# Optimization experiments

Hardware: AMD Instinct MI355X
Metric: run time of the kernel (lower is better)

## Reference

```python
import jax, jax.numpy as jnp
import numpy as np

MAX_ITER = 10
TAU = 1.0


def setup_inputs() -> dict:
    key = jax.random.key(0)
    k1, k2, k3 = jax.random.split(key, 3)
    B, R, C = 64, 1024, 1024
    s = jax.random.normal(k1, (B, R, C), dtype=jnp.float32)
    # nrows <= ncols per batch => no transposed_batch branch in the original
    nrows = jax.random.randint(k2, (B,), 128, 512).astype(jnp.int32)
    ncols = jax.random.randint(k3, (B,), 512, C + 1).astype(jnp.int32)
    return {"s": s, "nrows": nrows, "ncols": ncols}


def _masked_lse(x, mask, axis):
    """logsumexp over `axis` restricted to mask==True; finite-safe everywhere.
    Equivalent to torch.logsumexp after writing -inf into masked-out entries,
    but keeps all values finite so grads are clean."""
    neg = jnp.asarray(-1e30, x.dtype)
    m = jax.lax.stop_gradient(jnp.max(jnp.where(mask, x, neg), axis=axis, keepdims=True))
    e = jnp.where(mask, jnp.exp(jnp.where(mask, x, m) - m), jnp.zeros((), x.dtype))
    sum_e = jnp.sum(e, axis=axis, keepdims=True)
    any_m = jnp.any(mask, axis=axis, keepdims=True)
    return m + jnp.log(jnp.where(any_m, sum_e, jnp.ones((), x.dtype)))


def _sinkhorn(s, nrows, ncols):
    B, R, C = s.shape
    row_mask = (jnp.arange(R)[None, :] < nrows[:, None])[:, :, None]  # [B,R,1]
    col_mask = (jnp.arange(C)[None, :] < ncols[:, None])[:, None, :]  # [B,1,C]
    valid = row_mask & col_mask                                        # [B,R,C]
    log_s = s / TAU
    # Alternating row/col normalization in log space. In the original, entries
    # outside [nrows,ncols] are set to -inf and ignored by logsumexp; here we
    # keep them finite and mask inside the logsumexp, which is the same math
    # on the valid region, and we zero the invalid region at the end (exp(-inf)=0).
    for i in range(MAX_ITER):
        if i % 2 == 0:  # row normalization
            lse = _masked_lse(log_s, valid, axis=2)          # [B,R,1]
            log_s = log_s - jnp.where(row_mask, lse, 0.0)
        else:           # col normalization
            lse = _masked_lse(log_s, valid, axis=1)          # [B,1,C]
            log_s = log_s - jnp.where(col_mask, lse, 0.0)
    return jnp.where(valid, jnp.exp(log_s), jnp.zeros((), s.dtype))


def reference(s, nrows, ncols):
    return _sinkhorn(s, nrows, ncols)
```

## Files before the change

kernel.cpp:

```cpp
#include <hip/hip_runtime.h>
#include <hip/hip_fp16.h>


#define B_DIM 64

__device__ __forceinline__ float fast_rcp(float x) {
#if __has_builtin(__builtin_amdgcn_rcpf)
    return __builtin_amdgcn_rcpf(x);
#else
    return 1.0f / x;
#endif
}


__global__ __launch_bounds__(256) void pack_row0(
    const float* __restrict__ s, const int* __restrict__ nrows,
    const int* __restrict__ ncols, __half* __restrict__ E,
    float* __restrict__ a, float* __restrict__ cs0)
{
    const int b = blockIdx.y;
    const int t = threadIdx.x;
    if (blockIdx.x == 0) {
        #pragma unroll
        for (int k = 0; k < 4; ++k) cs0[(b << 10) + (k << 8) + t] = 0.f;
    }
    const int r = (blockIdx.x << 2) + (t >> 6);
    const int nr = nrows[b];
    if (r >= nr) return;
    const int lane = t & 63;
    const int nc = ncols[b];
    const float* __restrict__ srow = s + ((size_t)b << 20) + ((size_t)r << 10);
    __half* __restrict__ erow = E + ((size_t)b << 19) + ((size_t)r << 10);

    float sum = 0.f;
    #pragma unroll
    for (int k = 0; k < 4; ++k) {
        const int c = (k << 8) + (lane << 2);
        const float4 x = *reinterpret_cast<const float4*>(srow + c);
        const float e0 = __expf(x.x), e1 = __expf(x.y),
                    e2 = __expf(x.z), e3 = __expf(x.w);
        float2 pk;
        reinterpret_cast<__half2*>(&pk)[0] = __floats2half2_rn(e0, e1);
        reinterpret_cast<__half2*>(&pk)[1] = __floats2half2_rn(e2, e3);
        *reinterpret_cast<float2*>(erow + c) = pk;
        sum += (c + 0 < nc ? e0 : 0.f) + (c + 1 < nc ? e1 : 0.f)
             + (c + 2 < nc ? e2 : 0.f) + (c + 3 < nc ? e3 : 0.f);
    }
    #pragma unroll
    for (int off = 1; off < 64; off <<= 1) sum += __shfl_xor(sum, off);
    if (lane == 0) a[(b << 9) + r] = 1.0f / sum;
}

__global__ __launch_bounds__(256) void row_step_f(
    const __half* __restrict__ E, const int* __restrict__ nrows,
    const int* __restrict__ ncols, const float* __restrict__ cs_prev,
    float* __restrict__ cs_zero, float* __restrict__ a)
{
    const int b = blockIdx.y;
    const int t = threadIdx.x;
    if (blockIdx.x == 0) {
        #pragma unroll
        for (int k = 0; k < 4; ++k) cs_zero[(b << 10) + (k << 8) + t] = 0.f;
    }
    const int r = (blockIdx.x << 2) + (t >> 6);
    const int nr = nrows[b];
    if (r >= nr) return;
    const int lane = t & 63;
    const int nc = ncols[b];
    const __half* __restrict__ erow = E + ((size_t)b << 19) + ((size_t)r << 10);
    const float* __restrict__ csb = cs_prev + (b << 10);

    float sum = 0.f;
    #pragma unroll
    for (int k = 0; k < 4; ++k) {
        const int c = (k << 8) + (lane << 2);
        float2 pk = *reinterpret_cast<const float2*>(erow + c);
        const float2 f01 = __half22float2(reinterpret_cast<const __half2*>(&pk)[0]);
        const float2 f23 = __half22float2(reinterpret_cast<const __half2*>(&pk)[1]);
        const float4 cs = *reinterpret_cast<const float4*>(csb + c);
        const float w0 = (c + 0 < nc) ? fast_rcp(cs.x) : 0.f;
        const float w1 = (c + 1 < nc) ? fast_rcp(cs.y) : 0.f;
        const float w2 = (c + 2 < nc) ? fast_rcp(cs.z) : 0.f;
        const float w3 = (c + 3 < nc) ? fast_rcp(cs.w) : 0.f;
        sum += f01.x * w0 + f01.y * w1 + f23.x * w2 + f23.y * w3;
    }
    #pragma unroll
    for (int off = 1; off < 64; off <<= 1) sum += __shfl_xor(sum, off);
    if (lane == 0) a[(b << 9) + r] = 1.0f / sum;
}

__global__ __launch_bounds__(256) void col_step_f(
    const __half* __restrict__ E, const int* __restrict__ nrows,
    const int* __restrict__ ncols, const float* __restrict__ a,
    float* __restrict__ cs_out)
{
    const int b = blockIdx.z;
    const int nr = nrows[b];
    const int r0 = blockIdx.y << 6;
    if (r0 >= nr) return;
    const int nc = ncols[b];
    const int c0 = (blockIdx.x << 9) + (threadIdx.x << 1);
    if (c0 >= nc) return;
    const int rend = min(r0 + 64, nr);

    const __half* __restrict__ Eb = E + ((size_t)b << 19) + c0;
    const float* __restrict__ ab = a + (b << 9);

    float sA0 = 0.f, sA1 = 0.f, sB0 = 0.f, sB1 = 0.f;
    int r = r0;
    for (; r + 4 <= rend; r += 4) {
        const float2 f0 = __half22float2(*reinterpret_cast<const __half2*>(Eb + ((size_t)(r + 0) << 10)));
        const float2 f1 = __half22float2(*reinterpret_cast<const __half2*>(Eb + ((size_t)(r + 1) << 10)));
        const float2 f2 = __half22float2(*reinterpret_cast<const __half2*>(Eb + ((size_t)(r + 2) << 10)));
        const float2 f3 = __half22float2(*reinterpret_cast<const __half2*>(Eb + ((size_t)(r + 3) << 10)));
        const float a0 = ab[r + 0], a1 = ab[r + 1], a2 = ab[r + 2], a3 = ab[r + 3];
        sA0 = fmaf(f0.x, a0, sA0); sA1 = fmaf(f0.y, a0, sA1);
        sB0 = fmaf(f1.x, a1, sB0); sB1 = fmaf(f1.y, a1, sB1);
        sA0 = fmaf(f2.x, a2, sA0); sA1 = fmaf(f2.y, a2, sA1);
        sB0 = fmaf(f3.x, a3, sB0); sB1 = fmaf(f3.y, a3, sB1);
    }
    for (; r < rend; ++r) {
        const float2 f = __half22float2(*reinterpret_cast<const __half2*>(Eb + ((size_t)r << 10)));
        const float av = ab[r];
        sA0 = fmaf(f.x, av, sA0); sA1 = fmaf(f.y, av, sA1);
    }
    atomicAdd(cs_out + (b << 10) + c0, sA0 + sB0);
    if (c0 + 1 < nc)
        atomicAdd(cs_out + (b << 10) + c0 + 1, sA1 + sB1);
}

__global__ __launch_bounds__(256) void out_step_f(
    const __half* __restrict__ E, const int* __restrict__ nrows,
    const int* __restrict__ ncols, const float* __restrict__ a,
    const float* __restrict__ cs, float* __restrict__ out)
{
    const int g = (blockIdx.x << 8) + threadIdx.x;
    const int b = g >> 18;
    const int rem = g & 262143;
    const int r = rem >> 8;
    const int c0 = (rem & 255) << 2;
    const int nr = nrows[b];
    const int nc = ncols[b];
    float4 o = make_float4(0.f, 0.f, 0.f, 0.f);
    if (r < nr && c0 < nc) {
        const float ar = a[(b << 9) + r];
        float2 pk = *reinterpret_cast<const float2*>(
            E + ((size_t)b << 19) + ((size_t)r << 10) + c0);
        const float2 f01 = __half22float2(reinterpret_cast<const __half2*>(&pk)[0]);
        const float2 f23 = __half22float2(reinterpret_cast<const __half2*>(&pk)[1]);
        const float4 c4 = *reinterpret_cast<const float4*>(cs + (b << 10) + c0);
        o.x = f01.x * ar * fast_rcp(c4.x);
        o.y = (c0 + 1 < nc) ? f01.y * ar * fast_rcp(c4.y) : 0.f;
        o.z = (c0 + 2 < nc) ? f23.x * ar * fast_rcp(c4.z) : 0.f;
        o.w = (c0 + 3 < nc) ? f23.y * ar * fast_rcp(c4.w) : 0.f;
    }
    reinterpret_cast<float4*>(out)[g] = o;
}


__global__ __launch_bounds__(256) void row_step_lg(
    const float* __restrict__ s, const int* __restrict__ nrows,
    const int* __restrict__ ncols, const float* __restrict__ vlog,
    const int use_v, float* __restrict__ u)
{
    const int b = blockIdx.y, r = blockIdx.x;
    const int nr = nrows[b];
    if (r >= nr) return;
    const int nc = ncols[b];
    const int t = threadIdx.x, c0 = t << 2;
    float sum = 0.f;
    if (c0 < nc) {
        const float4 x = reinterpret_cast<const float4*>(
            s + ((size_t)b << 20) + ((size_t)r << 10))[t];
        float4 vv = make_float4(0.f, 0.f, 0.f, 0.f);
        if (use_v) vv = reinterpret_cast<const float4*>(vlog + ((size_t)b << 10))[t];
        sum  = (c0 + 0 < nc) ? __expf(x.x - vv.x) : 0.f;
        sum += (c0 + 1 < nc) ? __expf(x.y - vv.y) : 0.f;
        sum += (c0 + 2 < nc) ? __expf(x.z - vv.z) : 0.f;
        sum += (c0 + 3 < nc) ? __expf(x.w - vv.w) : 0.f;
    }
    #pragma unroll
    for (int off = 1; off < 64; off <<= 1) sum += __shfl_xor(sum, off);
    __shared__ float ss[4];
    if ((t & 63) == 0) ss[t >> 6] = sum;
    __syncthreads();
    if (t == 0) u[((size_t)b << 9) + r] = __logf(ss[0] + ss[1] + ss[2] + ss[3]);
}

__global__ __launch_bounds__(256) void col_step_lg(
    const float* __restrict__ s, const int* __restrict__ nrows,
    const int* __restrict__ ncols, const float* __restrict__ u,
    float* __restrict__ partial)
{
    const int b = blockIdx.z, rc = blockIdx.y;
    const int nr = nrows[b];
    const int r0 = rc << 6;
    if (r0 >= nr) return;
    const int nc = ncols[b];
    const int c = (blockIdx.x << 8) + threadIdx.x;
    float sum = 0.f;
    if (c < nc) {
        const int rend = min(r0 + 64, nr);
        const float* __restrict__ sb = s + ((size_t)b << 20) + c;
        const float* __restrict__ ub = u + ((size_t)b << 9);
        float s0 = 0.f, s1 = 0.f, s2 = 0.f, s3 = 0.f;
        int r = r0;
        for (; r + 4 <= rend; r += 4) {
            s0 += __expf(sb[(size_t)(r + 0) << 10] - ub[r + 0]);
            s1 += __expf(sb[(size_t)(r + 1) << 10] - ub[r + 1]);
            s2 += __expf(sb[(size_t)(r + 2) << 10] - ub[r + 2]);
            s3 += __expf(sb[(size_t)(r + 3) << 10] - ub[r + 3]);
        }
        for (; r < rend; ++r) s0 += __expf(sb[(size_t)r << 10] - ub[r]);
        sum = (s0 + s1) + (s2 + s3);
    }
    partial[(((size_t)b << 3) + rc) << 10 | c] = sum;
}

__global__ __launch_bounds__(256) void col_fin_lg(
    const int* __restrict__ nrows, const float* __restrict__ partial,
    float* __restrict__ vlog)
{
    const int idx = (blockIdx.x << 8) + threadIdx.x;
    const int b = idx >> 10;
    const int nch = (nrows[b] + 63) >> 6;
    const float* __restrict__ p = partial + ((size_t)(b << 3) << 10) + (idx & 1023);
    float sum = 0.f;
    for (int k = 0; k < nch; ++k) sum += p[(size_t)k << 10];
    vlog[idx] = (sum > 0.f) ? __logf(sum) : 0.f;
}

__global__ __launch_bounds__(256) void out_step_lg(
    const float* __restrict__ s, const int* __restrict__ nrows,
    const int* __restrict__ ncols, const float* __restrict__ u,
    const float* __restrict__ vlog, float* __restrict__ out)
{
    const size_t total4 = (size_t)B_DIM * 1024 * 1024 / 4;
    float4* out4 = reinterpret_cast<float4*>(out);
    const float4* s4 = reinterpret_cast<const float4*>(s);
    for (size_t i = (size_t)blockIdx.x * blockDim.x + threadIdx.x; i < total4;
         i += (size_t)gridDim.x * blockDim.x) {
        const int b = (int)(i >> 18);
        const int rem = (int)(i & 262143);
        const int r = rem >> 8;
        const int c0 = (rem & 255) << 2;
        const int nr = nrows[b], nc = ncols[b];
        float4 o;
        if (r >= nr || c0 >= nc) {
            o = make_float4(0.f, 0.f, 0.f, 0.f);
        } else {
            float4 x = s4[i];
            const float ur = u[((size_t)b << 9) + r];
            const float* vb = vlog + ((size_t)b << 10);
            o.x = (c0 + 0 < nc) ? __expf(x.x - ur - vb[c0 + 0]) : 0.f;
            o.y = (c0 + 1 < nc) ? __expf(x.y - ur - vb[c0 + 1]) : 0.f;
            o.z = (c0 + 2 < nc) ? __expf(x.z - ur - vb[c0 + 2]) : 0.f;
            o.w = (c0 + 3 < nc) ? __expf(x.w - ur - vb[c0 + 3]) : 0.f;
        }
        out4[i] = o;
    }
}


extern "C" void kernel_launch(void* const* d_in, const int* in_sizes, int n_in,
                              void* d_out, int out_size, void* d_ws, size_t ws_size,
                              hipStream_t stream) {
    const float* s = (const float*)d_in[0];
    const int* nrows = (const int*)d_in[1];
    const int* ncols = (const int*)d_in[2];
    float* out = (float*)d_out;

    const size_t E_BYTES = (size_t)B_DIM * 512 * 1024 * 2;
    const size_t NEED = E_BYTES + (size_t)B_DIM * 512 * 4 + 2 * (size_t)B_DIM * 1024 * 4;

    if (ws_size >= NEED) {
        __half* E = (__half*)d_ws;
        float* a = (float*)((char*)d_ws + E_BYTES);
        float* cs0 = a + B_DIM * 512;
        float* cs1 = cs0 + B_DIM * 1024;
        float* cs[2] = {cs0, cs1};

        const dim3 rowGrid(128, B_DIM);
        const dim3 colGrid(2, 8, B_DIM);
        pack_row0<<<rowGrid, 256, 0, stream>>>(s, nrows, ncols, E, a, cs0);
        col_step_f<<<colGrid, 256, 0, stream>>>(E, nrows, ncols, a, cs0);
        for (int i = 1; i < 5; ++i) {
            row_step_f<<<rowGrid, 256, 0, stream>>>(E, nrows, ncols,
                                                    cs[(i - 1) & 1], cs[i & 1], a);
            col_step_f<<<colGrid, 256, 0, stream>>>(E, nrows, ncols, a, cs[i & 1]);
        }
        out_step_f<<<65536, 256, 0, stream>>>(E, nrows, ncols, a, cs0, out);
    } else {
        float* u = (float*)d_ws;
        float* vlog = u + (size_t)B_DIM * 512;
        float* partial = vlog + (size_t)B_DIM * 1024;
        const dim3 rowGrid(512, B_DIM);
        const dim3 colGrid(4, 8, B_DIM);
        for (int it = 0; it < 5; ++it) {
            row_step_lg<<<rowGrid, 256, 0, stream>>>(s, nrows, ncols, vlog, it, u);
            col_step_lg<<<colGrid, 256, 0, stream>>>(s, nrows, ncols, u, partial);
            col_fin_lg<<<256, 256, 0, stream>>>(nrows, partial, vlog);
        }
        out_step_lg<<<4096, 256, 0, stream>>>(s, nrows, ncols, u, vlog, out);
    }
}
```

Before: 187.1 us.

## Fuse row and column Sinkhorn steps into one kernel per iteration pair

Merges each row-normalization kernel with the following column-sum kernel, so one block owns a 64-row chunk. It computes the row scales into LDS, then does the column partial sums with atomics from those rows, which it is likely to still find in cache. A third column-sum buffer and a memset rotate the zeroing so each launch clears the buffer for the next step. This halves the launch count, but the grid shrinks to 8x64 blocks of 512 threads, which may leave the GPU underoccupied.

```diff
diff --git a/kernel.cpp b/kernel.cpp
--- a/kernel.cpp
+++ b/kernel.cpp
@@ -12,99 +12,22 @@
 #endif
 }
 
-
-__global__ __launch_bounds__(256) void pack_row0(
-    const float* __restrict__ s, const int* __restrict__ nrows,
-    const int* __restrict__ ncols, __half* __restrict__ E,
-    float* __restrict__ a, float* __restrict__ cs0)
-{
-    const int b = blockIdx.y;
-    const int t = threadIdx.x;
-    if (blockIdx.x == 0) {
-        #pragma unroll
-        for (int k = 0; k < 4; ++k) cs0[(b << 10) + (k << 8) + t] = 0.f;
-    }
-    const int r = (blockIdx.x << 2) + (t >> 6);
-    const int nr = nrows[b];
-    if (r >= nr) return;
-    const int lane = t & 63;
-    const int nc = ncols[b];
-    const float* __restrict__ srow = s + ((size_t)b << 20) + ((size_t)r << 10);
-    __half* __restrict__ erow = E + ((size_t)b << 19) + ((size_t)r << 10);
-
-    float sum = 0.f;
+__device__ __forceinline__ float wave_sum(float x) {
     #pragma unroll
-    for (int k = 0; k < 4; ++k) {
-        const int c = (k << 8) + (lane << 2);
-        const float4 x = *reinterpret_cast<const float4*>(srow + c);
-        const float e0 = __expf(x.x), e1 = __expf(x.y),
-                    e2 = __expf(x.z), e3 = __expf(x.w);
-        float2 pk;
-        reinterpret_cast<__half2*>(&pk)[0] = __floats2half2_rn(e0, e1);
-        reinterpret_cast<__half2*>(&pk)[1] = __floats2half2_rn(e2, e3);
-        *reinterpret_cast<float2*>(erow + c) = pk;
-        sum += (c + 0 < nc ? e0 : 0.f) + (c + 1 < nc ? e1 : 0.f)
-             + (c + 2 < nc ? e2 : 0.f) + (c + 3 < nc ? e3 : 0.f);
-    }
-    #pragma unroll
-    for (int off = 1; off < 64; off <<= 1) sum += __shfl_xor(sum, off);
-    if (lane == 0) a[(b << 9) + r] = 1.0f / sum;
-}
-
-__global__ __launch_bounds__(256) void row_step_f(
-    const __half* __restrict__ E, const int* __restrict__ nrows,
-    const int* __restrict__ ncols, const float* __restrict__ cs_prev,
-    float* __restrict__ cs_zero, float* __restrict__ a)
-{
-    const int b = blockIdx.y;
-    const int t = threadIdx.x;
-    if (blockIdx.x == 0) {
-        #pragma unroll
-        for (int k = 0; k < 4; ++k) cs_zero[(b << 10) + (k << 8) + t] = 0.f;
-    }
-    const int r = (blockIdx.x << 2) + (t >> 6);
-    const int nr = nrows[b];
-    if (r >= nr) return;
-    const int lane = t & 63;
-    const int nc = ncols[b];
-    const __half* __restrict__ erow = E + ((size_t)b << 19) + ((size_t)r << 10);
-    const float* __restrict__ csb = cs_prev + (b << 10);
-
-    float sum = 0.f;
-    #pragma unroll
-    for (int k = 0; k < 4; ++k) {
-        const int c = (k << 8) + (lane << 2);
-        float2 pk = *reinterpret_cast<const float2*>(erow + c);
-        const float2 f01 = __half22float2(reinterpret_cast<const __half2*>(&pk)[0]);
-        const float2 f23 = __half22float2(reinterpret_cast<const __half2*>(&pk)[1]);
-        const float4 cs = *reinterpret_cast<const float4*>(csb + c);
-        const float w0 = (c + 0 < nc) ? fast_rcp(cs.x) : 0.f;
-        const float w1 = (c + 1 < nc) ? fast_rcp(cs.y) : 0.f;
-        const float w2 = (c + 2 < nc) ? fast_rcp(cs.z) : 0.f;
-        const float w3 = (c + 3 < nc) ? fast_rcp(cs.w) : 0.f;
-        sum += f01.x * w0 + f01.y * w1 + f23.x * w2 + f23.y * w3;
-    }
-    #pragma unroll
-    for (int off = 1; off < 64; off <<= 1) sum += __shfl_xor(sum, off);
-    if (lane == 0) a[(b << 9) + r] = 1.0f / sum;
-}
-
-__global__ __launch_bounds__(256) void col_step_f(
-    const __half* __restrict__ E, const int* __restrict__ nrows,
-    const int* __restrict__ ncols, const float* __restrict__ a,
-    float* __restrict__ cs_out)
-{
-    const int b = blockIdx.z;
-    const int nr = nrows[b];
-    const int r0 = blockIdx.y << 6;
+    for (int off = 1; off < 64; off <<= 1) x += __shfl_xor(x, off);
+    return x;
+}
+
+
+__device__ __forceinline__ void phase2_col(
+    const __half* __restrict__ E, const float* a_lds, int b, int r0, int nr,
+    int nc, int t, float* __restrict__ cs_cur)
+{
     if (r0 >= nr) return;
-    const int nc = ncols[b];
-    const int c0 = (blockIdx.x << 9) + (threadIdx.x << 1);
+    const int c0 = t << 1;
     if (c0 >= nc) return;
     const int rend = min(r0 + 64, nr);
-
     const __half* __restrict__ Eb = E + ((size_t)b << 19) + c0;
-    const float* __restrict__ ab = a + (b << 9);
 
     float sA0 = 0.f, sA1 = 0.f, sB0 = 0.f, sB1 = 0.f;
     int r = r0;
@@ -113,7 +36,8 @@
         const float2 f1 = __half22float2(*reinterpret_cast<const __half2*>(Eb + ((size_t)(r + 1) << 10)));
         const float2 f2 = __half22float2(*reinterpret_cast<const __half2*>(Eb + ((size_t)(r + 2) << 10)));
         const float2 f3 = __half22float2(*reinterpret_cast<const __half2*>(Eb + ((size_t)(r + 3) << 10)));
-        const float a0 = ab[r + 0], a1 = ab[r + 1], a2 = ab[r + 2], a3 = ab[r + 3];
+        const float a0 = a_lds[r + 0 - r0], a1 = a_lds[r + 1 - r0];
+        const float a2 = a_lds[r + 2 - r0], a3 = a_lds[r + 3 - r0];
         sA0 = fmaf(f0.x, a0, sA0); sA1 = fmaf(f0.y, a0, sA1);
         sB0 = fmaf(f1.x, a1, sB0); sB1 = fmaf(f1.y, a1, sB1);
         sA0 = fmaf(f2.x, a2, sA0); sA1 = fmaf(f2.y, a2, sA1);
@@ -121,12 +45,141 @@
     }
     for (; r < rend; ++r) {
         const float2 f = __half22float2(*reinterpret_cast<const __half2*>(Eb + ((size_t)r << 10)));
-        const float av = ab[r];
+        const float av = a_lds[r - r0];
         sA0 = fmaf(f.x, av, sA0); sA1 = fmaf(f.y, av, sA1);
     }
-    atomicAdd(cs_out + (b << 10) + c0, sA0 + sB0);
+    atomicAdd(cs_cur + (b << 10) + c0, sA0 + sB0);
     if (c0 + 1 < nc)
-        atomicAdd(cs_out + (b << 10) + c0 + 1, sA1 + sB1);
+        atomicAdd(cs_cur + (b << 10) + c0 + 1, sA1 + sB1);
+}
+
+__global__ __launch_bounds__(512) void pair_first(
+    const float* __restrict__ s, const int* __restrict__ nrows,
+    const int* __restrict__ ncols, __half* __restrict__ E,
+    float* __restrict__ a, float* __restrict__ cs_cur,
+    float* __restrict__ cs_next)
+{
+    const int b = blockIdx.y;
+    const int rc = blockIdx.x;
+    const int t = threadIdx.x;
+    if (t < 128) cs_next[(b << 10) + (rc << 7) + t] = 0.f;
+
+    const int nr = nrows[b];
+    const int nc = ncols[b];
+    const int r0 = rc << 6;
+    __shared__ float a_lds[64];
+
+    const int wave = t >> 6;
+    const int lane = t & 63;
+    const int cbase = lane << 4;
+    const int nv = min(max(nc - cbase, 0), 16);
+
+    if (r0 < nr) {
+        #pragma unroll 1
+        for (int k = 0; k < 8; ++k) {
+            const int r = r0 + (wave << 3) + k;
+            float s0 = 0.f, s1 = 0.f;
+            if (r < nr) {
+                const float* __restrict__ srow =
+                    s + ((size_t)b << 20) + ((size_t)r << 10) + cbase;
+                __half* __restrict__ erow =
+                    E + ((size_t)b << 19) + ((size_t)r << 10) + cbase;
+                float e[16];
+                #pragma unroll
+                for (int q = 0; q < 4; ++q) {
+                    const float4 x = *reinterpret_cast<const float4*>(srow + (q << 2));
+                    e[4 * q + 0] = __expf(x.x); e[4 * q + 1] = __expf(x.y);
+                    e[4 * q + 2] = __expf(x.z); e[4 * q + 3] = __expf(x.w);
+                }
+                __half2 h[8];
+                #pragma unroll
+                for (int q = 0; q < 8; ++q)
+                    h[q] = __floats2half2_rn(e[2 * q], e[2 * q + 1]);
+                *reinterpret_cast<float4*>(erow)     = *reinterpret_cast<float4*>(&h[0]);
+                *reinterpret_cast<float4*>(erow + 8) = *reinterpret_cast<float4*>(&h[4]);
+                #pragma unroll
+                for (int j = 0; j < 16; j += 2) {
+                    s0 += (j < nv) ? e[j] : 0.f;
+                    s1 += (j + 1 < nv) ? e[j + 1] : 0.f;
+                }
+            }
+            const float sum = wave_sum(s0 + s1);
+            if (lane == 0) a_lds[(wave << 3) + k] = (r < nr) ? 1.0f / sum : 0.f;
+        }
+    } else if (t < 64) {
+        a_lds[t] = 0.f;
+    }
+    __syncthreads();
+    if (t < 64) a[(b << 9) + r0 + t] = a_lds[t];
+
+    phase2_col(E, a_lds, b, r0, nr, nc, t, cs_cur);
+}
+
+__global__ __launch_bounds__(512) void pair_mid(
+    const __half* __restrict__ E, const int* __restrict__ nrows,
+    const int* __restrict__ ncols, const float* __restrict__ cs_prev,
+    float* __restrict__ a, float* __restrict__ cs_cur,
+    float* __restrict__ cs_next)
+{
+    const int b = blockIdx.y;
+    const int rc = blockIdx.x;
+    const int t = threadIdx.x;
+    if (t < 128) cs_next[(b << 10) + (rc << 7) + t] = 0.f;
+
+    const int nr = nrows[b];
+    const int nc = ncols[b];
+    const int r0 = rc << 6;
+    __shared__ float a_lds[64];
+
+    const int wave = t >> 6;
+    const int lane = t & 63;
+    const int cbase = lane << 4;
+
+    if (r0 < nr) {
+        float w[16];
+        const float* __restrict__ csp = cs_prev + (b << 10) + cbase;
+        #pragma unroll
+        for (int q = 0; q < 4; ++q) {
+            const float4 c4 = *reinterpret_cast<const float4*>(csp + (q << 2));
+            w[4 * q + 0] = (cbase + 4 * q + 0 < nc) ? fast_rcp(c4.x) : 0.f;
+            w[4 * q + 1] = (cbase + 4 * q + 1 < nc) ? fast_rcp(c4.y) : 0.f;
+            w[4 * q + 2] = (cbase + 4 * q + 2 < nc) ? fast_rcp(c4.z) : 0.f;
+            w[4 * q + 3] = (cbase + 4 * q + 3 < nc) ? fast_rcp(c4.w) : 0.f;
+        }
+        #pragma unroll 1
+        for (int k = 0; k < 8; ++k) {
+            const int r = r0 + (wave << 3) + k;
+            float s0 = 0.f, s1 = 0.f;
+            if (r < nr) {
+                const __half* __restrict__ erow =
+                    E + ((size_t)b << 19) + ((size_t)r << 10) + cbase;
+                float4 p0 = *reinterpret_cast<const float4*>(erow);
+                float4 p1 = *reinterpret_cast<const float4*>(erow + 8);
+                const __half2* h0 = reinterpret_cast<const __half2*>(&p0);
+                const __half2* h1 = reinterpret_cast<const __half2*>(&p1);
+                #pragma unroll
+                for (int q = 0; q < 4; ++q) {
+                    const float2 f = __half22float2(h0[q]);
+                    s0 = fmaf(f.x, w[2 * q], s0);
+                    s1 = fmaf(f.y, w[2 * q + 1], s1);
+                }
+                #pragma unroll
+                for (int q = 0; q < 4; ++q) {
+                    const float2 f = __half22float2(h1[q]);
+                    s0 = fmaf(f.x, w[8 + 2 * q], s0);
+                    s1 = fmaf(f.y, w[8 + 2 * q + 1], s1);
+                }
+            }
+            const float sum = wave_sum(s0 + s1);
+            if (lane == 0) a_lds[(wave << 3) + k] = (r < nr) ? 1.0f / sum : 0.f;
+        }
+    } else if (t < 64) {
+        a_lds[t] = 0.f;
+    }
+    __syncthreads();
+    if (t < 64) a[(b << 9) + r0 + t] = a_lds[t];
+
+    phase2_col(E, a_lds, b, r0, nr, nc, t, cs_cur);
 }
 
 __global__ __launch_bounds__(256) void out_step_f(
@@ -271,25 +324,25 @@
     float* out = (float*)d_out;
 
     const size_t E_BYTES = (size_t)B_DIM * 512 * 1024 * 2;
-    const size_t NEED = E_BYTES + (size_t)B_DIM * 512 * 4 + 2 * (size_t)B_DIM * 1024 * 4;
+    const size_t CS_ELEMS = (size_t)B_DIM * 1024;
+    const size_t NEED = E_BYTES + (size_t)B_DIM * 512 * 4 + 3 * CS_ELEMS * 4;
 
     if (ws_size >= NEED) {
         __half* E = (__half*)d_ws;
         float* a = (float*)((char*)d_ws + E_BYTES);
         float* cs0 = a + B_DIM * 512;
-        float* cs1 = cs0 + B_DIM * 1024;
-        float* cs[2] = {cs0, cs1};
-
-        const dim3 rowGrid(128, B_DIM);
-        const dim3 colGrid(2, 8, B_DIM);
-        pack_row0<<<rowGrid, 256, 0, stream>>>(s, nrows, ncols, E, a, cs0);
-        col_step_f<<<colGrid, 256, 0, stream>>>(E, nrows, ncols, a, cs0);
-        for (int i = 1; i < 5; ++i) {
-            row_step_f<<<rowGrid, 256, 0, stream>>>(E, nrows, ncols,
-                                                    cs[(i - 1) & 1], cs[i & 1], a);
-            col_step_f<<<colGrid, 256, 0, stream>>>(E, nrows, ncols, a, cs[i & 1]);
-        }
-        out_step_f<<<65536, 256, 0, stream>>>(E, nrows, ncols, a, cs0, out);
+        float* cs1 = cs0 + CS_ELEMS;
+        float* cs2 = cs1 + CS_ELEMS;
+
+        hipMemsetAsync(cs0, 0, CS_ELEMS * sizeof(float), stream);
+
+        const dim3 grid(8, B_DIM);
+        pair_first<<<grid, 512, 0, stream>>>(s, nrows, ncols, E, a, cs0, cs1);
+        pair_mid<<<grid, 512, 0, stream>>>(E, nrows, ncols, cs0, a, cs1, cs2);
+        pair_mid<<<grid, 512, 0, stream>>>(E, nrows, ncols, cs1, a, cs2, cs0);
+        pair_mid<<<grid, 512, 0, stream>>>(E, nrows, ncols, cs2, a, cs0, cs1);
+        pair_mid<<<grid, 512, 0, stream>>>(E, nrows, ncols, cs0, a, cs1, cs2);
+        out_step_f<<<65536, 256, 0, stream>>>(E, nrows, ncols, a, cs1, out);
     } else {
         float* u = (float*)d_ws;
         float* vlog = u + (size_t)B_DIM * 512;
```

Result: no change. 190.6 us (+1.9%).
